# Optimization experiments

Measured on AMD Instinct MI355X. Metric: run time of the kernel, lower is better.

## Reference

```python
import jax, jax.numpy as jnp
import numpy as np

N = 100000
E = 1600000
H = 8
C = 16
DIM = 128
EDGE_DIM = 32


def setup_inputs() -> dict:
    key = jax.random.key(0)
    ks = jax.random.split(key, 7)
    s = 1.0 / np.sqrt(DIM)
    return {
        "x": jax.random.normal(ks[0], (N, DIM), dtype=jnp.float32),
        "edge_index": jax.random.randint(ks[1], (2, E), 0, N, dtype=jnp.int32),
        "edge_attr": jax.random.normal(ks[2], (E, EDGE_DIM), dtype=jnp.float32),
        "Wq": jax.random.normal(ks[3], (H * C, DIM), dtype=jnp.float32) * s,
        "Wk": jax.random.normal(ks[4], (H * C, DIM), dtype=jnp.float32) * s,
        "Wv": jax.random.normal(ks[5], (H * C, DIM), dtype=jnp.float32) * s,
        "We": jax.random.normal(ks[6], (H, EDGE_DIM), dtype=jnp.float32) * (1.0 / np.sqrt(EDGE_DIM)),
    }


def reference(x, edge_index, edge_attr, Wq, Wk, Wv, We):
    # Node projections: [N, H, C]
    q = (x @ Wq.T).reshape(N, H, C)
    k = (x @ Wk.T).reshape(N, H, C)
    v = (x @ Wv.T).reshape(N, H, C)

    src, dst = edge_index[0], edge_index[1]

    # Per-edge attention logits with edge bias: [E, H]
    edge_bias = edge_attr @ We.T
    scores = jnp.einsum("ehc,ehc->eh", q[dst], k[src]) / np.sqrt(C) + edge_bias

    # Numerically-stable segment softmax over destination groups
    seg_max = jax.ops.segment_max(scores, dst, num_segments=N)  # [N, H]
    ex = jnp.exp(scores - seg_max[dst])
    denom = jax.ops.segment_sum(ex, dst, num_segments=N)  # [N, H]
    alpha = ex / denom[dst]  # [E, H]

    # Scale gathered values and scatter-add to destinations
    msgs = v[src] * alpha[:, :, None]  # [E, H, C]
    out = jax.ops.segment_sum(msgs, dst, num_segments=N)  # [N, H, C]
    return out.reshape(N, H * C)
```

## Files before the change

### kernel.cpp

```cpp
#include <hip/hip_runtime.h>


typedef unsigned int uint32;
typedef unsigned short ushort16;

__device__ inline unsigned short f2bf(float f) {
    uint32 u = __float_as_uint(f);
    uint32 r = u + 0x7fffu + ((u >> 16) & 1u);
    return (unsigned short)(r >> 16);
}

__global__ __launch_bounds__(256) void qkv_count_kernel(
    const float* __restrict__ x,
    const float* __restrict__ Wq,
    const float* __restrict__ Wk,
    const float* __restrict__ Wv,
    const int* __restrict__ edge_index,
    float* __restrict__ q,
    unsigned short* __restrict__ kbf,
    unsigned short* __restrict__ vbf,
    int* __restrict__ counts,
    int N, int E)
{
    if (blockIdx.y == 6) {
        int idx = blockIdx.x * 256 + threadIdx.x;
        if (idx * 4 + 3 < E) {
            int4 d4 = ((const int4*)(edge_index + E))[idx];
            atomicAdd(&counts[d4.x], 1);
            atomicAdd(&counts[d4.y], 1);
            atomicAdd(&counts[d4.z], 1);
            atomicAdd(&counts[d4.w], 1);
        } else {
            for (int e = idx * 4; e < E; ++e)
                atomicAdd(&counts[edge_index[(size_t)E + e]], 1);
        }
        return;
    }

    const int nb = blockIdx.x * 64;
    const int cb = blockIdx.y * 64;
    const float* __restrict__ W = (cb < 128) ? Wq : (cb < 256) ? Wk : Wv;
    const int wrow0 = cb & 127;

    __shared__ float As[16][68];
    __shared__ float Bs[16][68];

    const int tid = threadIdx.x;
    const int tx = tid & 15;
    const int ty = tid >> 4;

    float acc[4][4] = {};

    const int lrow = tid >> 2;
    const int lk   = (tid & 3) * 4;
    const int n_load = nb + lrow;

    for (int k0 = 0; k0 < 128; k0 += 16) {
        float4 a = make_float4(0.f, 0.f, 0.f, 0.f);
        if (n_load < N)
            a = *(const float4*)(x + (size_t)n_load * 128 + k0 + lk);
        float4 b = *(const float4*)(W + (size_t)(wrow0 + lrow) * 128 + k0 + lk);
        As[lk + 0][lrow] = a.x; As[lk + 1][lrow] = a.y;
        As[lk + 2][lrow] = a.z; As[lk + 3][lrow] = a.w;
        Bs[lk + 0][lrow] = b.x; Bs[lk + 1][lrow] = b.y;
        Bs[lk + 2][lrow] = b.z; Bs[lk + 3][lrow] = b.w;
        __syncthreads();
#pragma unroll
        for (int kk = 0; kk < 16; ++kk) {
            float4 av = *(const float4*)&As[kk][ty * 4];
            float4 bv = *(const float4*)&Bs[kk][tx * 4];
            float avr[4] = {av.x, av.y, av.z, av.w};
            float bvr[4] = {bv.x, bv.y, bv.z, bv.w};
#pragma unroll
            for (int i = 0; i < 4; ++i)
#pragma unroll
                for (int j = 0; j < 4; ++j)
                    acc[i][j] = fmaf(avr[i], bvr[j], acc[i][j]);
        }
        __syncthreads();
    }

#pragma unroll
    for (int i = 0; i < 4; ++i) {
        int n = nb + ty * 4 + i;
        if (n >= N) continue;
        if (cb < 128) {
            float4 o = make_float4(acc[i][0], acc[i][1], acc[i][2], acc[i][3]);
            *(float4*)(q + (size_t)n * 128 + wrow0 + tx * 4) = o;
        } else {
            unsigned short* kv = (cb < 256) ? kbf : vbf;
            ushort4 o;
            o.x = f2bf(acc[i][0]); o.y = f2bf(acc[i][1]);
            o.z = f2bf(acc[i][2]); o.w = f2bf(acc[i][3]);
            *(ushort4*)(kv + (size_t)n * 128 + wrow0 + tx * 4) = o;
        }
    }
}

__global__ __launch_bounds__(256) void scan_pass1(
    const int* __restrict__ counts, int* __restrict__ blocksums, int N)
{
    __shared__ int red[256];
    int base = blockIdx.x * 512;
    int t = threadIdx.x;
    int s = 0;
    if (base + t < N)       s += counts[base + t];
    if (base + 256 + t < N) s += counts[base + 256 + t];
    red[t] = s;
    __syncthreads();
    for (int off = 128; off > 0; off >>= 1) {
        if (t < off) red[t] += red[t + off];
        __syncthreads();
    }
    if (t == 0) blocksums[blockIdx.x] = red[0];
}

__global__ __launch_bounds__(256) void scan_pass2(
    const int* __restrict__ blocksums, int* __restrict__ blockbase, int NB)
{
    __shared__ int sc[256];
    int t = threadIdx.x;
    int v = (t < NB) ? blocksums[t] : 0;
    sc[t] = v;
    __syncthreads();
    for (int off = 1; off < 256; off <<= 1) {
        int tmp = (t >= off) ? sc[t - off] : 0;
        __syncthreads();
        sc[t] += tmp;
        __syncthreads();
    }
    if (t < NB) blockbase[t] = sc[t] - v;
}

__global__ __launch_bounds__(256) void scan_pass3(
    const int* __restrict__ counts, const int* __restrict__ blockbase,
    int* __restrict__ offsets, int* __restrict__ cursor, int N)
{
    __shared__ int sc[256];
    int base = blockIdx.x * 512;
    int t = threadIdx.x;
    int i0 = base + 2 * t, i1 = i0 + 1;
    int c0 = (i0 < N) ? counts[i0] : 0;
    int c1 = (i1 < N) ? counts[i1] : 0;
    int pair = c0 + c1;
    sc[t] = pair;
    __syncthreads();
    for (int off = 1; off < 256; off <<= 1) {
        int tmp = (t >= off) ? sc[t - off] : 0;
        __syncthreads();
        sc[t] += tmp;
        __syncthreads();
    }
    int ex = sc[t] - pair + blockbase[blockIdx.x];
    if (i0 < N) { offsets[i0] = ex;      cursor[i0] = ex; }
    if (i1 < N) { offsets[i1] = ex + c0; cursor[i1] = ex + c0; }
}

__global__ __launch_bounds__(256) void scatter_kernel(
    const int* __restrict__ edge_index,
    int* __restrict__ cursor,
    int2* __restrict__ perm,
    int E)
{
    int e = blockIdx.x * 256 + threadIdx.x;
    if (e >= E) return;
    int s = edge_index[e];
    int d = edge_index[(size_t)E + e];
    int pos = atomicAdd(&cursor[d], 1);
    perm[pos] = make_int2(s, e);
}

__global__ __launch_bounds__(256) void attn_fused_kernel(
    const float* __restrict__ q,
    const unsigned short* __restrict__ kbf,
    const unsigned short* __restrict__ vbf,
    const float* __restrict__ edge_attr,
    const float* __restrict__ We,
    const int* __restrict__ offsets,
    const int* __restrict__ counts,
    const int2* __restrict__ perm,
    float* __restrict__ out,
    int N)
{
    const int d    = blockIdx.x * 4 + (threadIdx.x >> 6);
    const int lane = threadIdx.x & 63;
    if (d >= N) return;
    const int h = lane >> 3;
    const int j = lane & 7;

    const float4 we4 = *(const float4*)(We + h * 32 + j * 4);
    const float2 q2  = *(const float2*)(q + (size_t)d * 128 + lane * 2);

    const int start = offsets[d];
    const int cnt   = counts[d];

    float denom = 0.f, accx = 0.f, accy = 0.f;

    for (int i0 = 0; i0 < cnt; i0 += 64) {
        int m = min(64, cnt - i0);
        int2 pv = make_int2(0, 0);
        if (lane < m) pv = perm[start + i0 + lane];

        int src = __shfl(pv.x, 0), e = __shfl(pv.y, 0);
        uint32 kk2 = *(const uint32*)(kbf + (size_t)src * 128 + lane * 2);
        uint32 vv2 = *(const uint32*)(vbf + (size_t)src * 128 + lane * 2);
        float4 ea  = *(const float4*)(edge_attr + (size_t)e * 32 + j * 4);

        for (int t = 0; t < m; ++t) {
            uint32 ck = kk2, cv = vv2;
            float4 cea = ea;
            if (t + 1 < m) {
                int ns = __shfl(pv.x, t + 1), ne = __shfl(pv.y, t + 1);
                kk2 = *(const uint32*)(kbf + (size_t)ns * 128 + lane * 2);
                vv2 = *(const uint32*)(vbf + (size_t)ns * 128 + lane * 2);
                ea  = *(const float4*)(edge_attr + (size_t)ne * 32 + j * 4);
            }
            float kx = __uint_as_float(ck << 16);
            float ky = __uint_as_float(ck & 0xffff0000u);
            float part = 0.25f * (q2.x * kx + q2.y * ky)
                       + cea.x * we4.x + cea.y * we4.y
                       + cea.z * we4.z + cea.w * we4.w;
            part += __shfl_xor(part, 1);
            part += __shfl_xor(part, 2);
            part += __shfl_xor(part, 4);
            float ev = __expf(part);
            denom += ev;
            float vx = __uint_as_float(cv << 16);
            float vy = __uint_as_float(cv & 0xffff0000u);
            accx = fmaf(ev, vx, accx);
            accy = fmaf(ev, vy, accy);
        }
    }

    float inv = denom > 0.f ? 1.f / denom : 0.f;
    *(float2*)(out + (size_t)d * 128 + lane * 2) = make_float2(accx * inv, accy * inv);
}

extern "C" void kernel_launch(void* const* d_in, const int* in_sizes, int n_in,
                              void* d_out, int out_size, void* d_ws, size_t ws_size,
                              hipStream_t stream) {
    const float* x          = (const float*)d_in[0];
    const int*   edge_index = (const int*)d_in[1];
    const float* edge_attr  = (const float*)d_in[2];
    const float* Wq         = (const float*)d_in[3];
    const float* Wk         = (const float*)d_in[4];
    const float* Wv         = (const float*)d_in[5];
    const float* We         = (const float*)d_in[6];
    float* out = (float*)d_out;

    const int N = in_sizes[0] / 128;
    const int E = in_sizes[1] / 2;

    float* q = (float*)d_ws;
    unsigned short* kbf = (unsigned short*)(q + (size_t)N * 128);
    unsigned short* vbf = kbf + (size_t)N * 128;
    int2* perm = (int2*)(vbf + (size_t)N * 128);
    int* counts    = (int*)(perm + E);
    int* offsets   = counts + N;
    int* cursor    = offsets + N;
    int* blocksums = cursor + N;
    int* blockbase = blocksums + 256;

    hipMemsetAsync(counts, 0, (size_t)N * sizeof(int), stream);

    const int nxb = (N + 63) / 64;
    dim3 g1(nxb, 7);
    qkv_count_kernel<<<g1, 256, 0, stream>>>(x, Wq, Wk, Wv, edge_index,
                                             q, kbf, vbf, counts, N, E);

    const int NB = (N + 511) / 512;
    scan_pass1<<<NB, 256, 0, stream>>>(counts, blocksums, N);
    scan_pass2<<<1, 256, 0, stream>>>(blocksums, blockbase, NB);
    scan_pass3<<<NB, 256, 0, stream>>>(counts, blockbase, offsets, cursor, N);

    scatter_kernel<<<(E + 255) / 256, 256, 0, stream>>>(edge_index, cursor,
                                                        perm, E);

    attn_fused_kernel<<<(N + 3) / 4, 256, 0, stream>>>(
        q, kbf, vbf, edge_attr, We, offsets, counts, perm, out, N);
}
```

Baseline: 769.2 us.

## Precompute bf16 edge bias, store q in bf16, reuse x tile across QKV

Adds a kernel that computes the per-edge, per-head bias from edge_attr and We in a coalesced pass and stores it as bf16. The attention loop then gathers 2 bytes per lane instead of float4 chunks of edge_attr. q is also stored in bf16, and the projection kernel loads each x tile once into shared memory and loops over all six output tiles with double-buffered weight tiles. This cuts gather traffic and redundant x reloads, at the cost of reduced precision for q and the bias, plus an extra kernel launch.

```diff
diff --git a/kernel.cpp b/kernel.cpp
--- a/kernel.cpp
+++ b/kernel.cpp
@@ -2,12 +2,14 @@
 
 
 typedef unsigned int uint32;
-typedef unsigned short ushort16;
 
 __device__ inline unsigned short f2bf(float f) {
     uint32 u = __float_as_uint(f);
     uint32 r = u + 0x7fffu + ((u >> 16) & 1u);
     return (unsigned short)(r >> 16);
+}
+__device__ inline float bf2f(unsigned short b) {
+    return __uint_as_float(((uint32)b) << 16);
 }
 
 __global__ __launch_bounds__(256) void qkv_count_kernel(
@@ -16,13 +18,13 @@
     const float* __restrict__ Wk,
     const float* __restrict__ Wv,
     const int* __restrict__ edge_index,
-    float* __restrict__ q,
+    unsigned short* __restrict__ qbf,
     unsigned short* __restrict__ kbf,
     unsigned short* __restrict__ vbf,
     int* __restrict__ counts,
     int N, int E)
 {
-    if (blockIdx.y == 6) {
+    if (blockIdx.y == 1) {
         int idx = blockIdx.x * 256 + threadIdx.x;
         if (idx * 4 + 3 < E) {
             int4 d4 = ((const int4*)(edge_index + E))[idx];
@@ -38,62 +40,120 @@
     }
 
     const int nb = blockIdx.x * 64;
-    const int cb = blockIdx.y * 64;
-    const float* __restrict__ W = (cb < 128) ? Wq : (cb < 256) ? Wk : Wv;
-    const int wrow0 = cb & 127;
-
-    __shared__ float As[16][68];
-    __shared__ float Bs[16][68];
+    __shared__ float As[128][65];
+    __shared__ float Bs[2][16][68];
 
     const int tid = threadIdx.x;
+
+#pragma unroll
+    for (int r = 0; r < 8; ++r) {
+        int fid = tid + 256 * r;
+        int n  = fid >> 5;
+        int kq = (fid & 31) * 4;
+        float4 a = make_float4(0.f, 0.f, 0.f, 0.f);
+        if (nb + n < N)
+            a = *(const float4*)(x + (size_t)(nb + n) * 128 + kq);
+        As[kq + 0][n] = a.x; As[kq + 1][n] = a.y;
+        As[kq + 2][n] = a.z; As[kq + 3][n] = a.w;
+    }
+
     const int tx = tid & 15;
     const int ty = tid >> 4;
-
-    float acc[4][4] = {};
-
-    const int lrow = tid >> 2;
-    const int lk   = (tid & 3) * 4;
-    const int n_load = nb + lrow;
-
-    for (int k0 = 0; k0 < 128; k0 += 16) {
-        float4 a = make_float4(0.f, 0.f, 0.f, 0.f);
-        if (n_load < N)
-            a = *(const float4*)(x + (size_t)n_load * 128 + k0 + lk);
-        float4 b = *(const float4*)(W + (size_t)(wrow0 + lrow) * 128 + k0 + lk);
-        As[lk + 0][lrow] = a.x; As[lk + 1][lrow] = a.y;
-        As[lk + 2][lrow] = a.z; As[lk + 3][lrow] = a.w;
-        Bs[lk + 0][lrow] = b.x; Bs[lk + 1][lrow] = b.y;
-        Bs[lk + 2][lrow] = b.z; Bs[lk + 3][lrow] = b.w;
-        __syncthreads();
-#pragma unroll
-        for (int kk = 0; kk < 16; ++kk) {
-            float4 av = *(const float4*)&As[kk][ty * 4];
-            float4 bv = *(const float4*)&Bs[kk][tx * 4];
-            float avr[4] = {av.x, av.y, av.z, av.w};
-            float bvr[4] = {bv.x, bv.y, bv.z, bv.w};
-#pragma unroll
-            for (int i = 0; i < 4; ++i)
-#pragma unroll
-                for (int j = 0; j < 4; ++j)
-                    acc[i][j] = fmaf(avr[i], bvr[j], acc[i][j]);
-        }
-        __syncthreads();
-    }
-
-#pragma unroll
-    for (int i = 0; i < 4; ++i) {
-        int n = nb + ty * 4 + i;
-        if (n >= N) continue;
-        if (cb < 128) {
-            float4 o = make_float4(acc[i][0], acc[i][1], acc[i][2], acc[i][3]);
-            *(float4*)(q + (size_t)n * 128 + wrow0 + tx * 4) = o;
-        } else {
-            unsigned short* kv = (cb < 256) ? kbf : vbf;
+    const int brow = tid >> 2;
+    const int bk   = (tid & 3) * 4;
+
+    for (int cb = 0; cb < 6; ++cb) {
+        const float* __restrict__ W = (cb < 2) ? Wq : (cb < 4) ? Wk : Wv;
+        const int wrow0 = (cb & 1) * 64;
+        float acc[4][4] = {};
+
+        {
+            float4 b = *(const float4*)(W + (size_t)(wrow0 + brow) * 128 + bk);
+            __syncthreads();
+            Bs[0][bk + 0][brow] = b.x; Bs[0][bk + 1][brow] = b.y;
+            Bs[0][bk + 2][brow] = b.z; Bs[0][bk + 3][brow] = b.w;
+        }
+        __syncthreads();
+
+        for (int t0 = 0; t0 < 8; ++t0) {
+            int cur = t0 & 1;
+            if (t0 + 1 < 8) {
+                int nxt = cur ^ 1;
+                float4 b = *(const float4*)(W + (size_t)(wrow0 + brow) * 128 +
+                                            (t0 + 1) * 16 + bk);
+                Bs[nxt][bk + 0][brow] = b.x; Bs[nxt][bk + 1][brow] = b.y;
+                Bs[nxt][bk + 2][brow] = b.z; Bs[nxt][bk + 3][brow] = b.w;
+            }
+#pragma unroll
+            for (int kk = 0; kk < 16; ++kk) {
+                float av[4];
+#pragma unroll
+                for (int i = 0; i < 4; ++i) av[i] = As[t0 * 16 + kk][ty * 4 + i];
+                float4 bv = *(const float4*)&Bs[cur][kk][tx * 4];
+                float bvr[4] = {bv.x, bv.y, bv.z, bv.w};
+#pragma unroll
+                for (int i = 0; i < 4; ++i)
+#pragma unroll
+                    for (int j = 0; j < 4; ++j)
+                        acc[i][j] = fmaf(av[i], bvr[j], acc[i][j]);
+            }
+            __syncthreads();
+        }
+
+        unsigned short* __restrict__ dst =
+            (cb < 2) ? qbf : (cb < 4) ? kbf : vbf;
+#pragma unroll
+        for (int i = 0; i < 4; ++i) {
+            int n = nb + ty * 4 + i;
+            if (n >= N) continue;
             ushort4 o;
             o.x = f2bf(acc[i][0]); o.y = f2bf(acc[i][1]);
             o.z = f2bf(acc[i][2]); o.w = f2bf(acc[i][3]);
-            *(ushort4*)(kv + (size_t)n * 128 + wrow0 + tx * 4) = o;
-        }
+            *(ushort4*)(dst + (size_t)n * 128 + wrow0 + tx * 4) = o;
+        }
+    }
+}
+
+__global__ __launch_bounds__(256) void edge_bias_kernel(
+    const float* __restrict__ edge_attr,
+    const float* __restrict__ We,
+    unsigned short* __restrict__ bias16,
+    int E)
+{
+    __shared__ float eaS[64][33];
+    __shared__ float WeS[8][33];
+
+    const int tid = threadIdx.x;
+    if (tid < 256) {
+        int h = tid >> 5, c = tid & 31;
+        WeS[h][c] = We[h * 32 + c];
+    }
+
+    const int e0 = blockIdx.x * 64;
+#pragma unroll
+    for (int r = 0; r < 2; ++r) {
+        int fid = tid + 256 * r;
+        int el = fid >> 3;
+        int cq = (fid & 7) * 4;
+        float4 a = make_float4(0.f, 0.f, 0.f, 0.f);
+        if (e0 + el < E)
+            a = *(const float4*)(edge_attr + (size_t)(e0 + el) * 32 + cq);
+        eaS[el][cq + 0] = a.x; eaS[el][cq + 1] = a.y;
+        eaS[el][cq + 2] = a.z; eaS[el][cq + 3] = a.w;
+    }
+    __syncthreads();
+
+#pragma unroll
+    for (int r = 0; r < 2; ++r) {
+        int p = tid + 256 * r;
+        int el = p >> 3;
+        int h  = p & 7;
+        float s = 0.f;
+#pragma unroll
+        for (int c = 0; c < 32; ++c)
+            s = fmaf(eaS[el][c], WeS[h][c], s);
+        if (e0 + el < E)
+            bias16[(size_t)(e0 + el) * 8 + h] = f2bf(s);
     }
 }
 
@@ -171,11 +231,10 @@
 }
 
 __global__ __launch_bounds__(256) void attn_fused_kernel(
-    const float* __restrict__ q,
+    const unsigned short* __restrict__ qbf,
     const unsigned short* __restrict__ kbf,
     const unsigned short* __restrict__ vbf,
-    const float* __restrict__ edge_attr,
-    const float* __restrict__ We,
+    const unsigned short* __restrict__ bias16,
     const int* __restrict__ offsets,
     const int* __restrict__ counts,
     const int2* __restrict__ perm,
@@ -186,10 +245,10 @@
     const int lane = threadIdx.x & 63;
     if (d >= N) return;
     const int h = lane >> 3;
-    const int j = lane & 7;
-
-    const float4 we4 = *(const float4*)(We + h * 32 + j * 4);
-    const float2 q2  = *(const float2*)(q + (size_t)d * 128 + lane * 2);
+
+    uint32 qq = *(const uint32*)(qbf + (size_t)d * 128 + lane * 2);
+    const float qx = __uint_as_float(qq << 16);
+    const float qy = __uint_as_float(qq & 0xffff0000u);
 
     const int start = offsets[d];
     const int cnt   = counts[d];
@@ -204,31 +263,27 @@
         int src = __shfl(pv.x, 0), e = __shfl(pv.y, 0);
         uint32 kk2 = *(const uint32*)(kbf + (size_t)src * 128 + lane * 2);
         uint32 vv2 = *(const uint32*)(vbf + (size_t)src * 128 + lane * 2);
-        float4 ea  = *(const float4*)(edge_attr + (size_t)e * 32 + j * 4);
+        unsigned short bb = bias16[(size_t)e * 8 + h];
 
         for (int t = 0; t < m; ++t) {
             uint32 ck = kk2, cv = vv2;
-            float4 cea = ea;
+            unsigned short cbb = bb;
             if (t + 1 < m) {
                 int ns = __shfl(pv.x, t + 1), ne = __shfl(pv.y, t + 1);
                 kk2 = *(const uint32*)(kbf + (size_t)ns * 128 + lane * 2);
                 vv2 = *(const uint32*)(vbf + (size_t)ns * 128 + lane * 2);
-                ea  = *(const float4*)(edge_attr + (size_t)ne * 32 + j * 4);
+                bb  = bias16[(size_t)ne * 8 + h];
             }
             float kx = __uint_as_float(ck << 16);
             float ky = __uint_as_float(ck & 0xffff0000u);
-            float part = 0.25f * (q2.x * kx + q2.y * ky)
-                       + cea.x * we4.x + cea.y * we4.y
-                       + cea.z * we4.z + cea.w * we4.w;
+            float part = qx * kx + qy * ky;
             part += __shfl_xor(part, 1);
             part += __shfl_xor(part, 2);
             part += __shfl_xor(part, 4);
-            float ev = __expf(part);
+            float ev = __expf(fmaf(0.25f, part, bf2f(cbb)));
             denom += ev;
-            float vx = __uint_as_float(cv << 16);
-            float vy = __uint_as_float(cv & 0xffff0000u);
-            accx = fmaf(ev, vx, accx);
-            accy = fmaf(ev, vy, accy);
+            accx = fmaf(ev, __uint_as_float(cv << 16), accx);
+            accy = fmaf(ev, __uint_as_float(cv & 0xffff0000u), accy);
         }
     }
 
@@ -251,10 +306,11 @@
     const int N = in_sizes[0] / 128;
     const int E = in_sizes[1] / 2;
 
-    float* q = (float*)d_ws;
-    unsigned short* kbf = (unsigned short*)(q + (size_t)N * 128);
+    unsigned short* qbf = (unsigned short*)d_ws;
+    unsigned short* kbf = qbf + (size_t)N * 128;
     unsigned short* vbf = kbf + (size_t)N * 128;
-    int2* perm = (int2*)(vbf + (size_t)N * 128);
+    unsigned short* bias16 = vbf + (size_t)N * 128;
+    int2* perm = (int2*)(bias16 + (size_t)E * 8);
     int* counts    = (int*)(perm + E);
     int* offsets   = counts + N;
     int* cursor    = offsets + N;
@@ -264,9 +320,12 @@
     hipMemsetAsync(counts, 0, (size_t)N * sizeof(int), stream);
 
     const int nxb = (N + 63) / 64;
-    dim3 g1(nxb, 7);
+    dim3 g1(nxb, 2);
     qkv_count_kernel<<<g1, 256, 0, stream>>>(x, Wq, Wk, Wv, edge_index,
-                                             q, kbf, vbf, counts, N, E);
+                                             qbf, kbf, vbf, counts, N, E);
+
+    edge_bias_kernel<<<(E + 63) / 64, 256, 0, stream>>>(edge_attr, We,
+                                                        bias16, E);
 
     const int NB = (N + 511) / 512;
     scan_pass1<<<NB, 256, 0, stream>>>(counts, blocksums, N);
@@ -277,5 +336,5 @@
                                                         perm, E);
 
     attn_fused_kernel<<<(N + 3) / 4, 256, 0, stream>>>(
-        q, kbf, vbf, edge_attr, We, offsets, counts, perm, out, N);
-}
+        qbf, kbf, vbf, bias16, offsets, counts, perm, out, N);
+}
```

New measurement: 837.6 us. 1.09x slower.
